# Kernel tuning notes

Measured on AMD Instinct MI355X. Metric: run time of the kernel, lower is better.

The kernel has to match this reference:

```python
import jax, jax.numpy as jnp
import numpy as np

N = 10000      # nodes
E = 100000     # edges
C = 32         # in_channels == hidden_channels == out_channels
ED = 4         # edge_dim
G = 64         # number of graphs in the batch
EPS = 1e-5     # BatchNorm eps


def setup_inputs() -> dict:
    key = jax.random.key(0)
    ks = jax.random.split(key, 20)
    rn = lambda k, shape, s=0.05: jax.random.normal(k, shape, dtype=jnp.float32) * s
    return {
        "x": jax.random.normal(ks[0], (N, C), dtype=jnp.float32),
        "edge_attr": jax.random.normal(ks[1], (E, ED), dtype=jnp.float32),
        # edge MLP 1: ED -> C -> C*C ; NNConv1 root/bias
        "e1_w1": rn(ks[2], (ED, C)), "e1_b1": jnp.zeros((C,), jnp.float32),
        "e1_w2": rn(ks[3], (C, C * C)), "e1_b2": jnp.zeros((C * C,), jnp.float32),
        "root1": rn(ks[4], (C, C)), "bias1": jnp.zeros((C,), jnp.float32),
        # edge MLP 2: ED -> C -> C*C ; NNConv2 root/bias
        "e2_w1": rn(ks[5], (ED, C)), "e2_b1": jnp.zeros((C,), jnp.float32),
        "e2_w2": rn(ks[6], (C, C * C)), "e2_b2": jnp.zeros((C * C,), jnp.float32),
        "root2": rn(ks[7], (C, C)), "bias2": jnp.zeros((C,), jnp.float32),
        # BatchNorm (eval mode: running stats)
        "bn1_g": jnp.ones((C,), jnp.float32), "bn1_b": jnp.zeros((C,), jnp.float32),
        "bn1_m": rn(ks[8], (C,), 0.1), "bn1_v": 1.0 + 0.1 * jax.random.uniform(ks[9], (C,), dtype=jnp.float32),
        "bn2_g": jnp.ones((C,), jnp.float32), "bn2_b": jnp.zeros((C,), jnp.float32),
        "bn2_m": rn(ks[10], (C,), 0.1), "bn2_v": 1.0 + 0.1 * jax.random.uniform(ks[11], (C,), dtype=jnp.float32),
        # readout: C -> C//2 -> 1
        "r1_w": rn(ks[12], (C, C // 2)), "r1_b": jnp.zeros((C // 2,), jnp.float32),
        "r2_w": rn(ks[13], (C // 2, 1)), "r2_b": jnp.zeros((1,), jnp.float32),
        "edge_index": jax.random.randint(ks[14], (2, E), 0, N),
        "batch": jnp.sort(jax.random.randint(ks[15], (N,), 0, G)),
    }


def _nnconv(x, edge_index, edge_attr, w1, b1, w2, b2, root, bias):
    # edge MLP -> per-edge weight matrix [E, C, C]
    h = jax.nn.relu(edge_attr @ w1 + b1)
    W = (h @ w2 + b2).reshape(E, C, C)
    src, dst = edge_index[0], edge_index[1]
    # gather source features, per-edge matmul, scatter-mean to target nodes
    msg = jnp.einsum('ei,eio->eo', x[src], W)                      # [E, C]
    agg = jax.ops.segment_sum(msg, dst, num_segments=N)            # [N, C]
    cnt = jax.ops.segment_sum(jnp.ones((E,), x.dtype), dst, num_segments=N)
    agg = agg / jnp.maximum(cnt, 1.0)[:, None]
    return agg + x @ root + bias


def _bn(x, g, b, m, v):
    return (x - m) * jax.lax.rsqrt(v + EPS) * g + b


def reference(x, edge_attr,
              e1_w1, e1_b1, e1_w2, e1_b2, root1, bias1,
              e2_w1, e2_b1, e2_w2, e2_b2, root2, bias2,
              bn1_g, bn1_b, bn1_m, bn1_v,
              bn2_g, bn2_b, bn2_m, bn2_v,
              r1_w, r1_b, r2_w, r2_b,
              edge_index, batch):
    h = jax.nn.relu(_bn(_nnconv(x, edge_index, edge_attr, e1_w1, e1_b1, e1_w2, e1_b2, root1, bias1),
                        bn1_g, bn1_b, bn1_m, bn1_v))
    h = jax.nn.relu(_bn(_nnconv(h, edge_index, edge_attr, e2_w1, e2_b1, e2_w2, e2_b2, root2, bias2),
                        bn2_g, bn2_b, bn2_m, bn2_v))
    # global mean pool over graphs
    psum = jax.ops.segment_sum(h, batch, num_segments=G)           # [G, C]
    pcnt = jax.ops.segment_sum(jnp.ones((N,), h.dtype), batch, num_segments=G)
    pooled = psum / jnp.maximum(pcnt, 1.0)[:, None]
    # readout MLP (dropout is identity in eval)
    return jax.nn.relu(pooled @ r1_w + r1_b) @ r2_w + r2_b          # [G, 1]
```

## Files before the change

kernel.cpp:

```cpp
#include <hip/hip_runtime.h>

#define NN 10000
#define EE 100000
#define GG 64
#define EPSV 1e-5f
#define SLOTS 1056
#define PST 36
#define PNODE (32*PST)
#define HBLK 391
#define WBLK 160
#define NBK 1250

#define OFF_W2R1   0
#define OFF_W2R2   135168
#define OFF_MSG1   270336
#define OFF_MSG2   13070336
#define OFF_EACSR  25870336
#define OFF_CNT    27470336
#define OFF_DEG    27510336
#define OFF_PSUM   27550336
#define OFF_DONE   27558528
#define OFF_XMID   27558592
#define OFF_ROWPTR 28838592
#define OFF_CURSOR 28878656
#define OFF_COLPTR 28918656
#define OFF_CCUR   28958720
#define OFF_MSRC   28998720
#define OFF_CPOS   29398720

__global__ __launch_bounds__(256) void k_pre(const int* __restrict__ ei,
        int* __restrict__ cnt, int* __restrict__ deg,
        const float* __restrict__ w2a, const float* __restrict__ b2a,
        const float* __restrict__ w2b, const float* __restrict__ b2b,
        float* __restrict__ w2r1, float* __restrict__ w2r2) {
    int blk = blockIdx.x;
    int t = threadIdx.x;
    if (blk < HBLK) {
        int e = blk * 256 + t;
        if (e < EE) {
            atomicAdd(&cnt[ei[EE + e]], 1);
            atomicAdd(&deg[ei[e]], 1);
        }
    } else {
        int b2i = blk - HBLK;
        int s = (b2i % 5) * 256 + t;
        int i = b2i / 5;
        if (s < SLOTS) {
            float va = (s < 1024) ? w2a[(s >> 5) * 1024 + i * 32 + (s & 31)]
                                  : b2a[i * 32 + (s - 1024)];
            float vb = (s < 1024) ? w2b[(s >> 5) * 1024 + i * 32 + (s & 31)]
                                  : b2b[i * 32 + (s - 1024)];
            w2r1[i * SLOTS + s] = va;
            w2r2[i * SLOTS + s] = vb;
        }
    }
}

__global__ __launch_bounds__(1024) void k_scan2(const int* __restrict__ deg,
                                                const int* __restrict__ cnt,
                                                int* __restrict__ rowptr,
                                                int* __restrict__ cursor,
                                                int* __restrict__ colptr,
                                                int* __restrict__ ccursor) {
    __shared__ int buf[1024];
    int pass = blockIdx.x;
    const int* src = pass ? cnt : deg;
    int* dst_p = pass ? colptr : rowptr;
    int* dst_c = pass ? ccursor : cursor;
    int t = threadIdx.x;
    int base = t * 10;
    int v[10]; int s = 0;
    #pragma unroll
    for (int k = 0; k < 10; k++) {
        int idx = base + k;
        v[k] = (idx < NN) ? src[idx] : 0;
        s += v[k];
    }
    buf[t] = s;
    for (int off = 1; off < 1024; off <<= 1) {
        __syncthreads();
        int val = buf[t] + ((t >= off) ? buf[t - off] : 0);
        __syncthreads();
        buf[t] = val;
    }
    __syncthreads();
    int carry = (t > 0) ? buf[t - 1] : 0;
    #pragma unroll
    for (int k = 0; k < 10; k++) {
        int idx = base + k;
        if (idx < NN) { dst_p[idx] = carry; dst_c[idx] = carry; }
        carry += v[k];
    }
    if (t == 1023) dst_p[NN] = buf[1023];
}

__global__ void k_scatter(const int* __restrict__ ei,
        const float* __restrict__ edge_attr,
        int* __restrict__ cursor, int* __restrict__ ccursor,
        int* __restrict__ msrc, int* __restrict__ cpos,
        float4* __restrict__ ea_csr) {
    int e = blockIdx.x * 256 + threadIdx.x;
    if (e >= EE) return;
    int sn = ei[e];
    int dn = ei[EE + e];
    float4 a = *(const float4*)&edge_attr[(size_t)e * 4];
    int pos = atomicAdd(&cursor[sn], 1);
    msrc[pos] = sn;
    ea_csr[pos] = a;
    int cp = atomicAdd(&ccursor[dn], 1);
    cpos[cp] = pos;
}

__global__ __launch_bounds__(256, 3) void k_f1(const float* __restrict__ x,
        const float4* __restrict__ ea_csr,
        const float* __restrict__ w1, const float* __restrict__ b1,
        const float* __restrict__ w2r,
        const int* __restrict__ msrc, const int* __restrict__ rowptr,
        float* __restrict__ msg) {
    __shared__ float xs[8][32];
    __shared__ float P2[8 * PNODE];
    __shared__ float shx[8][32];
    int t = threadIdx.x;
    int o = t & 31;
    int cb = 4 * (t >> 5);
    int n0 = blockIdx.x * 8;

    int ebase = rowptr[n0];
    int eend  = rowptr[n0 + 8];
    int grp = t >> 5;

    float wc0 = w1[o], wc1 = w1[32 + o], wc2 = w1[64 + o], wc3 = w1[96 + o];
    float bb  = b1[o];

    int pos = ebase + grp;
    float4 aC = make_float4(0.f, 0.f, 0.f, 0.f);
    int srcC = n0;
    if (pos < eend) { aC = ea_csr[pos]; srcC = msrc[pos]; }

    xs[grp][o] = x[n0 * 32 + t];
    __syncthreads();

    {
        float acc[4][8];
        #pragma unroll
        for (int k = 0; k < 4; k++)
            #pragma unroll
            for (int n = 0; n < 8; n++) acc[k][n] = 0.f;
        #pragma unroll
        for (int j = 0; j < 8; j++) {
            float wk[4][4];
            #pragma unroll
            for (int r = 0; r < 4; r++)
                #pragma unroll
                for (int k = 0; k < 4; k++)
                    wk[r][k] = w2r[(4 * j + r) * SLOTS + (cb + k) * 32 + o];
            #pragma unroll
            for (int n = 0; n < 8; n++) {
                float4 xq = *(const float4*)&xs[n][4 * j];
                #pragma unroll
                for (int k = 0; k < 4; k++)
                    acc[k][n] += xq.x * wk[0][k] + xq.y * wk[1][k]
                               + xq.z * wk[2][k] + xq.w * wk[3][k];
            }
        }
        #pragma unroll
        for (int n = 0; n < 8; n++) {
            float4 st = make_float4(acc[0][n], acc[1][n], acc[2][n], acc[3][n]);
            *(float4*)&P2[n * PNODE + o * PST + cb] = st;
        }
    }
    if (t < 32) {
        float wb[32];
        #pragma unroll
        for (int i = 0; i < 32; i++) wb[i] = w2r[i * SLOTS + 1024 + t];
        #pragma unroll
        for (int n = 0; n < 8; n++) {
            float b = 0.f;
            #pragma unroll
            for (int j = 0; j < 8; j++) {
                float4 xq = *(const float4*)&xs[n][4 * j];
                b += xq.x * wb[4 * j] + xq.y * wb[4 * j + 1]
                   + xq.z * wb[4 * j + 2] + xq.w * wb[4 * j + 3];
            }
            *(float4*)&P2[n * PNODE + t * PST + 32] = make_float4(b, 0.f, 0.f, 0.f);
        }
    }
    __syncthreads();

    while (pos < eend) {
        int pn = pos + 8;
        float4 aN = aC; int srcN = srcC;
        if (pn < eend) { aN = ea_csr[pn]; srcN = msrc[pn]; }
        float h = fmaxf(aC.x * wc0 + aC.y * wc1 + aC.z * wc2 + aC.w * wc3 + bb, 0.f);
        shx[grp][o] = h;
        asm volatile("" ::: "memory");
        const float* Pn = &P2[(srcC - n0) * PNODE + o * PST];
        float m = Pn[32];
        #pragma unroll
        for (int b = 0; b < 8; b++) {
            float4 hx = *(const float4*)&shx[grp][4 * b];
            float4 pq = *(const float4*)&Pn[4 * b];
            m += hx.x * pq.x + hx.y * pq.y + hx.z * pq.z + hx.w * pq.w;
        }
        msg[(size_t)pos * 32 + o] = m;
        asm volatile("" ::: "memory");
        pos = pn; aC = aN; srcC = srcN;
    }
}

__global__ __launch_bounds__(256, 3) void k_mid(const float* __restrict__ x,
        const float* __restrict__ msg1,
        const int* __restrict__ colptr, const int* __restrict__ cpos,
        const float* __restrict__ root1, const float* __restrict__ bias1,
        const float* __restrict__ bn1g, const float* __restrict__ bn1b,
        const float* __restrict__ bn1m, const float* __restrict__ bn1v,
        const float4* __restrict__ ea_csr,
        const float* __restrict__ w1, const float* __restrict__ b1,
        const float* __restrict__ w2r,
        const int* __restrict__ msrc, const int* __restrict__ rowptr,
        float* __restrict__ xmid, float* __restrict__ msg2) {
    __shared__ float xs[8][32];
    __shared__ float P2[8 * PNODE];
    __shared__ float shx[8][32];
    __shared__ float xmid_s[8][32];
    int t = threadIdx.x;
    int o = t & 31;
    int grp = t >> 5;
    int cb = 4 * grp;
    int n0 = blockIdx.x * 8;

    int ebase = rowptr[n0];
    int eend  = rowptr[n0 + 8];

    float wc0 = w1[o], wc1 = w1[32 + o], wc2 = w1[64 + o], wc3 = w1[96 + o];
    float hbb = b1[o];
    int pos = ebase + grp;
    float4 aC = make_float4(0.f, 0.f, 0.f, 0.f);
    int srcC = n0;
    if (pos < eend) { aC = ea_csr[pos]; srcC = msrc[pos]; }

    xs[grp][o] = x[n0 * 32 + t];
    __syncthreads();
    {
        int k = grp, n = n0 + k;
        float rt = bias1[o];
        #pragma unroll
        for (int i = 0; i < 32; i++) rt += xs[k][i] * root1[i * 32 + o];
        int jbase = colptr[n], jend = colptr[n + 1];
        float acc = 0.f;
        for (int jb = jbase; jb < jend; jb += 32) {
            int nrem = jend - jb;
            int lim = (nrem < 32) ? nrem : 32;
            int cv = 0;
            if (o < lim) cv = cpos[jb + o];
            for (int j = 0; j < lim; j += 8) {
                float v[8];
                #pragma unroll
                for (int q = 0; q < 8; q++) {
                    if (j + q < lim) {
                        int cj = __shfl(cv, j + q, 32);
                        v[q] = msg1[(size_t)cj * 32 + o];
                    } else v[q] = 0.f;
                }
                #pragma unroll
                for (int q = 0; q < 8; q++) acc += v[q];
            }
        }
        float a = acc / fmaxf((float)(jend - jbase), 1.f);
        float val = a + rt;
        val = (val - bn1m[o]) * rsqrtf(bn1v[o] + EPSV) * bn1g[o] + bn1b[o];
        val = fmaxf(val, 0.f);
        xmid_s[k][o] = val;
        xmid[(size_t)n * 32 + o] = val;
    }
    __syncthreads();

    {
        float acc[4][8];
        #pragma unroll
        for (int k = 0; k < 4; k++)
            #pragma unroll
            for (int n = 0; n < 8; n++) acc[k][n] = 0.f;
        #pragma unroll
        for (int j = 0; j < 8; j++) {
            float wk[4][4];
            #pragma unroll
            for (int r = 0; r < 4; r++)
                #pragma unroll
                for (int k = 0; k < 4; k++)
                    wk[r][k] = w2r[(4 * j + r) * SLOTS + (cb + k) * 32 + o];
            #pragma unroll
            for (int n = 0; n < 8; n++) {
                float4 xq = *(const float4*)&xmid_s[n][4 * j];
                #pragma unroll
                for (int k = 0; k < 4; k++)
                    acc[k][n] += xq.x * wk[0][k] + xq.y * wk[1][k]
                               + xq.z * wk[2][k] + xq.w * wk[3][k];
            }
        }
        #pragma unroll
        for (int n = 0; n < 8; n++) {
            float4 st = make_float4(acc[0][n], acc[1][n], acc[2][n], acc[3][n]);
            *(float4*)&P2[n * PNODE + o * PST + cb] = st;
        }
    }
    if (t < 32) {
        float wb[32];
        #pragma unroll
        for (int i = 0; i < 32; i++) wb[i] = w2r[i * SLOTS + 1024 + t];
        #pragma unroll
        for (int n = 0; n < 8; n++) {
            float b = 0.f;
            #pragma unroll
            for (int j = 0; j < 8; j++) {
                float4 xq = *(const float4*)&xmid_s[n][4 * j];
                b += xq.x * wb[4 * j] + xq.y * wb[4 * j + 1]
                   + xq.z * wb[4 * j + 2] + xq.w * wb[4 * j + 3];
            }
            *(float4*)&P2[n * PNODE + t * PST + 32] = make_float4(b, 0.f, 0.f, 0.f);
        }
    }
    __syncthreads();

    while (pos < eend) {
        int pn = pos + 8;
        float4 aN = aC; int srcN = srcC;
        if (pn < eend) { aN = ea_csr[pn]; srcN = msrc[pn]; }
        float h = fmaxf(aC.x * wc0 + aC.y * wc1 + aC.z * wc2 + aC.w * wc3 + hbb, 0.f);
        shx[grp][o] = h;
        asm volatile("" ::: "memory");
        const float* Pn = &P2[(srcC - n0) * PNODE + o * PST];
        float m = Pn[32];
        #pragma unroll
        for (int b = 0; b < 8; b++) {
            float4 hx = *(const float4*)&shx[grp][4 * b];
            float4 pq = *(const float4*)&Pn[4 * b];
            m += hx.x * pq.x + hx.y * pq.y + hx.z * pq.z + hx.w * pq.w;
        }
        msg2[(size_t)pos * 32 + o] = m;
        asm volatile("" ::: "memory");
        pos = pn; aC = aN; srcC = srcN;
    }
}

__global__ __launch_bounds__(256) void k_end(const float* __restrict__ xmid,
        const float* __restrict__ msg2,
        const int* __restrict__ colptr, const int* __restrict__ cpos,
        const float* __restrict__ root2, const float* __restrict__ bias2,
        const float* __restrict__ bn2g, const float* __restrict__ bn2b,
        const float* __restrict__ bn2m, const float* __restrict__ bn2v,
        const int* __restrict__ batch, float* __restrict__ psum,
        int* __restrict__ done,
        const float* __restrict__ r1w, const float* __restrict__ r1b,
        const float* __restrict__ r2w, const float* __restrict__ r2b,
        float* __restrict__ out) {
    __shared__ float xs[8][32];
    __shared__ float vals[8][32];
    __shared__ int gb[8];
    __shared__ float rd[2592];
    __shared__ int lastflag;
    int t = threadIdx.x;
    int o = t & 31;
    int grp = t >> 5;
    int n0 = blockIdx.x * 8;

    xs[grp][o] = xmid[(size_t)n0 * 32 + t];
    __syncthreads();
    int k = grp, n = n0 + k;
    float rt = bias2[o];
    #pragma unroll
    for (int i = 0; i < 32; i++) rt += xs[k][i] * root2[i * 32 + o];
    int jbase = colptr[n], jend = colptr[n + 1];
    float acc = 0.f;
    for (int jb = jbase; jb < jend; jb += 32) {
        int nrem = jend - jb;
        int lim = (nrem < 32) ? nrem : 32;
        int cv = 0;
        if (o < lim) cv = cpos[jb + o];
        for (int j = 0; j < lim; j += 8) {
            float v[8];
            #pragma unroll
            for (int q = 0; q < 8; q++) {
                if (j + q < lim) {
                    int cj = __shfl(cv, j + q, 32);
                    v[q] = msg2[(size_t)cj * 32 + o];
                } else v[q] = 0.f;
            }
            #pragma unroll
            for (int q = 0; q < 8; q++) acc += v[q];
        }
    }
    float a = acc / fmaxf((float)(jend - jbase), 1.f);
    float val = a + rt;
    val = (val - bn2m[o]) * rsqrtf(bn2v[o] + EPSV) * bn2g[o] + bn2b[o];
    val = fmaxf(val, 0.f);
    vals[k][o] = val;
    if (o == 0) gb[k] = batch[n];
    __syncthreads();
    if (k == 0) {
        float pacc = vals[0][o];
        int g = gb[0];
        #pragma unroll
        for (int k2 = 1; k2 < 8; k2++) {
            if (gb[k2] == g) pacc += vals[k2][o];
            else {
                atomicAdd(&psum[(size_t)g * 32 + o], pacc);
                g = gb[k2]; pacc = vals[k2][o];
            }
        }
        atomicAdd(&psum[(size_t)g * 32 + o], pacc);
    }
    __syncthreads();

    if (t == 0) {
        __threadfence();
        int old = atomicAdd(done, 1);
        lastflag = (old == NBK - 1);
    }
    __syncthreads();
    if (!lastflag) return;
    __threadfence();

    float* w1s = rd;
    float* b1s = rd + 512;
    float* w2s = rd + 528;
    float* ps  = rd + 544;
    int cnt_g = 0;
    if (t < GG) {
        int lo = 0, hi = NN;
        while (lo < hi) { int m2 = (lo + hi) >> 1; if (batch[m2] < t) lo = m2 + 1; else hi = m2; }
        int lb = lo;
        lo = 0; hi = NN;
        while (lo < hi) { int m2 = (lo + hi) >> 1; if (batch[m2] < t + 1) lo = m2 + 1; else hi = m2; }
        cnt_g = lo - lb;
    }
    w1s[t] = r1w[t];
    w1s[t + 256] = r1w[t + 256];
    if (t < 16) { b1s[t] = r1b[t]; w2s[t] = r2w[t]; }
    #pragma unroll
    for (int i = 0; i < GG * 32 / 256; i++)
        ps[t + i * 256] = __hip_atomic_load(&psum[t + i * 256], __ATOMIC_RELAXED,
                                            __HIP_MEMORY_SCOPE_AGENT);
    __syncthreads();
    if (t < GG) {
        float inv = 1.f / fmaxf((float)cnt_g, 1.f);
        float acc2 = r2b[0];
        #pragma unroll
        for (int j = 0; j < 16; j++) {
            float dot = 0.f;
            #pragma unroll
            for (int c = 0; c < 32; c++) dot += ps[t * 32 + c] * w1s[c * 16 + j];
            float z = dot * inv + b1s[j];
            acc2 += fmaxf(z, 0.f) * w2s[j];
        }
        out[t] = acc2;
    }
}

extern "C" void kernel_launch(void* const* d_in, const int* in_sizes, int n_in,
                              void* d_out, int out_size, void* d_ws, size_t ws_size,
                              hipStream_t stream) {
    const float* x       = (const float*)d_in[0];
    const float* eattr   = (const float*)d_in[1];
    const float* e1_w1   = (const float*)d_in[2];
    const float* e1_b1   = (const float*)d_in[3];
    const float* e1_w2   = (const float*)d_in[4];
    const float* e1_b2   = (const float*)d_in[5];
    const float* root1   = (const float*)d_in[6];
    const float* bias1   = (const float*)d_in[7];
    const float* e2_w1   = (const float*)d_in[8];
    const float* e2_b1   = (const float*)d_in[9];
    const float* e2_w2   = (const float*)d_in[10];
    const float* e2_b2   = (const float*)d_in[11];
    const float* root2   = (const float*)d_in[12];
    const float* bias2   = (const float*)d_in[13];
    const float* bn1_g   = (const float*)d_in[14];
    const float* bn1_b   = (const float*)d_in[15];
    const float* bn1_m   = (const float*)d_in[16];
    const float* bn1_v   = (const float*)d_in[17];
    const float* bn2_g   = (const float*)d_in[18];
    const float* bn2_b   = (const float*)d_in[19];
    const float* bn2_m   = (const float*)d_in[20];
    const float* bn2_v   = (const float*)d_in[21];
    const float* r1_w    = (const float*)d_in[22];
    const float* r1_b    = (const float*)d_in[23];
    const float* r2_w    = (const float*)d_in[24];
    const float* r2_b    = (const float*)d_in[25];
    const int*   ei      = (const int*)d_in[26];
    const int*   batch   = (const int*)d_in[27];

    char* ws = (char*)d_ws;
    float*  w2r1   = (float*) (ws + OFF_W2R1);
    float*  w2r2   = (float*) (ws + OFF_W2R2);
    float*  msg1   = (float*) (ws + OFF_MSG1);
    float*  msg2   = (float*) (ws + OFF_MSG2);
    float4* ea_csr = (float4*)(ws + OFF_EACSR);
    int*    cnt    = (int*)   (ws + OFF_CNT);
    int*    deg    = (int*)   (ws + OFF_DEG);
    float*  psum   = (float*) (ws + OFF_PSUM);
    int*    done   = (int*)   (ws + OFF_DONE);
    float*  xmid   = (float*) (ws + OFF_XMID);
    int*    rowptr = (int*)   (ws + OFF_ROWPTR);
    int*    cursor = (int*)   (ws + OFF_CURSOR);
    int*    colptr = (int*)   (ws + OFF_COLPTR);
    int*    ccursor= (int*)   (ws + OFF_CCUR);
    int*    msrc   = (int*)   (ws + OFF_MSRC);
    int*    cpos   = (int*)   (ws + OFF_CPOS);

    hipMemsetAsync(ws + OFF_CNT, 0, 88256, stream);

    k_pre<<<HBLK + WBLK, 256, 0, stream>>>(ei, cnt, deg,
                                           e1_w2, e1_b2, e2_w2, e2_b2, w2r1, w2r2);
    k_scan2<<<2, 1024, 0, stream>>>(deg, cnt, rowptr, cursor, colptr, ccursor);
    k_scatter<<<(EE + 255) / 256, 256, 0, stream>>>(ei, eattr,
                                                    cursor, ccursor, msrc, cpos,
                                                    ea_csr);

    k_f1<<<NBK, 256, 0, stream>>>(x, ea_csr, e1_w1, e1_b1, w2r1,
                                  msrc, rowptr, msg1);
    k_mid<<<NBK, 256, 0, stream>>>(x, msg1, colptr, cpos, root1, bias1,
                                   bn1_g, bn1_b, bn1_m, bn1_v,
                                   ea_csr, e2_w1, e2_b1, w2r2,
                                   msrc, rowptr, xmid, msg2);
    k_end<<<NBK, 256, 0, stream>>>(xmid, msg2, colptr, cpos, root2, bias2,
                                   bn2_g, bn2_b, bn2_m, bn2_v,
                                   batch, psum, done,
                                   r1_w, r1_b, r2_w, r2_b, (float*)d_out);
}
```

Before: 263.2 us.

## Write edge messages in destination-sorted order to make aggregation contiguous

```diff
diff --git a/kernel.cpp b/kernel.cpp
--- a/kernel.cpp
+++ b/kernel.cpp
@@ -25,8 +25,7 @@
 #define OFF_CURSOR 28878656
 #define OFF_COLPTR 28918656
 #define OFF_CCUR   28958720
-#define OFF_MSRC   28998720
-#define OFF_CPOS   29398720
+#define OFF_META   28998720
 
 __global__ __launch_bounds__(256) void k_pre(const int* __restrict__ ei,
         int* __restrict__ cnt, int* __restrict__ deg,
@@ -97,25 +96,23 @@
 __global__ void k_scatter(const int* __restrict__ ei,
         const float* __restrict__ edge_attr,
         int* __restrict__ cursor, int* __restrict__ ccursor,
-        int* __restrict__ msrc, int* __restrict__ cpos,
-        float4* __restrict__ ea_csr) {
+        int2* __restrict__ meta, float4* __restrict__ ea_csr) {
     int e = blockIdx.x * 256 + threadIdx.x;
     if (e >= EE) return;
     int sn = ei[e];
     int dn = ei[EE + e];
     float4 a = *(const float4*)&edge_attr[(size_t)e * 4];
     int pos = atomicAdd(&cursor[sn], 1);
-    msrc[pos] = sn;
+    int cs  = atomicAdd(&ccursor[dn], 1);
+    meta[pos] = make_int2(sn, cs);
     ea_csr[pos] = a;
-    int cp = atomicAdd(&ccursor[dn], 1);
-    cpos[cp] = pos;
 }
 
 __global__ __launch_bounds__(256, 3) void k_f1(const float* __restrict__ x,
         const float4* __restrict__ ea_csr,
         const float* __restrict__ w1, const float* __restrict__ b1,
         const float* __restrict__ w2r,
-        const int* __restrict__ msrc, const int* __restrict__ rowptr,
+        const int2* __restrict__ meta, const int* __restrict__ rowptr,
         float* __restrict__ msg) {
     __shared__ float xs[8][32];
     __shared__ float P2[8 * PNODE];
@@ -134,8 +131,8 @@
 
     int pos = ebase + grp;
     float4 aC = make_float4(0.f, 0.f, 0.f, 0.f);
-    int srcC = n0;
-    if (pos < eend) { aC = ea_csr[pos]; srcC = msrc[pos]; }
+    int2 mC = make_int2(n0, 0);
+    if (pos < eend) { aC = ea_csr[pos]; mC = meta[pos]; }
 
     xs[grp][o] = x[n0 * 32 + t];
     __syncthreads();
@@ -189,12 +186,12 @@
 
     while (pos < eend) {
         int pn = pos + 8;
-        float4 aN = aC; int srcN = srcC;
-        if (pn < eend) { aN = ea_csr[pn]; srcN = msrc[pn]; }
+        float4 aN = aC; int2 mN = mC;
+        if (pn < eend) { aN = ea_csr[pn]; mN = meta[pn]; }
         float h = fmaxf(aC.x * wc0 + aC.y * wc1 + aC.z * wc2 + aC.w * wc3 + bb, 0.f);
         shx[grp][o] = h;
         asm volatile("" ::: "memory");
-        const float* Pn = &P2[(srcC - n0) * PNODE + o * PST];
+        const float* Pn = &P2[(mC.x - n0) * PNODE + o * PST];
         float m = Pn[32];
         #pragma unroll
         for (int b = 0; b < 8; b++) {
@@ -202,22 +199,22 @@
             float4 pq = *(const float4*)&Pn[4 * b];
             m += hx.x * pq.x + hx.y * pq.y + hx.z * pq.z + hx.w * pq.w;
         }
-        msg[(size_t)pos * 32 + o] = m;
+        msg[(size_t)mC.y * 32 + o] = m;
         asm volatile("" ::: "memory");
-        pos = pn; aC = aN; srcC = srcN;
+        pos = pn; aC = aN; mC = mN;
     }
 }
 
 __global__ __launch_bounds__(256, 3) void k_mid(const float* __restrict__ x,
         const float* __restrict__ msg1,
-        const int* __restrict__ colptr, const int* __restrict__ cpos,
+        const int* __restrict__ colptr,
         const float* __restrict__ root1, const float* __restrict__ bias1,
         const float* __restrict__ bn1g, const float* __restrict__ bn1b,
         const float* __restrict__ bn1m, const float* __restrict__ bn1v,
         const float4* __restrict__ ea_csr,
         const float* __restrict__ w1, const float* __restrict__ b1,
         const float* __restrict__ w2r,
-        const int* __restrict__ msrc, const int* __restrict__ rowptr,
+        const int2* __restrict__ meta, const int* __restrict__ rowptr,
         float* __restrict__ xmid, float* __restrict__ msg2) {
     __shared__ float xs[8][32];
     __shared__ float P2[8 * PNODE];
@@ -236,8 +233,8 @@
     float hbb = b1[o];
     int pos = ebase + grp;
     float4 aC = make_float4(0.f, 0.f, 0.f, 0.f);
-    int srcC = n0;
-    if (pos < eend) { aC = ea_csr[pos]; srcC = msrc[pos]; }
+    int2 mC = make_int2(n0, 0);
+    if (pos < eend) { aC = ea_csr[pos]; mC = meta[pos]; }
 
     xs[grp][o] = x[n0 * 32 + t];
     __syncthreads();
@@ -248,24 +245,19 @@
         for (int i = 0; i < 32; i++) rt += xs[k][i] * root1[i * 32 + o];
         int jbase = colptr[n], jend = colptr[n + 1];
         float acc = 0.f;
-        for (int jb = jbase; jb < jend; jb += 32) {
-            int nrem = jend - jb;
-            int lim = (nrem < 32) ? nrem : 32;
-            int cv = 0;
-            if (o < lim) cv = cpos[jb + o];
-            for (int j = 0; j < lim; j += 8) {
-                float v[8];
-                #pragma unroll
-                for (int q = 0; q < 8; q++) {
-                    if (j + q < lim) {
-                        int cj = __shfl(cv, j + q, 32);
-                        v[q] = msg1[(size_t)cj * 32 + o];
-                    } else v[q] = 0.f;
-                }
-                #pragma unroll
-                for (int q = 0; q < 8; q++) acc += v[q];
-            }
-        }
+        int j = jbase;
+        for (; j + 8 <= jend; j += 8) {
+            float v0 = msg1[(size_t)(j + 0) * 32 + o];
+            float v1 = msg1[(size_t)(j + 1) * 32 + o];
+            float v2 = msg1[(size_t)(j + 2) * 32 + o];
+            float v3 = msg1[(size_t)(j + 3) * 32 + o];
+            float v4 = msg1[(size_t)(j + 4) * 32 + o];
+            float v5 = msg1[(size_t)(j + 5) * 32 + o];
+            float v6 = msg1[(size_t)(j + 6) * 32 + o];
+            float v7 = msg1[(size_t)(j + 7) * 32 + o];
+            acc += ((v0 + v1) + (v2 + v3)) + ((v4 + v5) + (v6 + v7));
+        }
+        for (; j < jend; j++) acc += msg1[(size_t)j * 32 + o];
         float a = acc / fmaxf((float)(jend - jbase), 1.f);
         float val = a + rt;
         val = (val - bn1m[o]) * rsqrtf(bn1v[o] + EPSV) * bn1g[o] + bn1b[o];
@@ -324,12 +316,12 @@
 
     while (pos < eend) {
         int pn = pos + 8;
-        float4 aN = aC; int srcN = srcC;
-        if (pn < eend) { aN = ea_csr[pn]; srcN = msrc[pn]; }
+        float4 aN = aC; int2 mN = mC;
+        if (pn < eend) { aN = ea_csr[pn]; mN = meta[pn]; }
         float h = fmaxf(aC.x * wc0 + aC.y * wc1 + aC.z * wc2 + aC.w * wc3 + hbb, 0.f);
         shx[grp][o] = h;
         asm volatile("" ::: "memory");
-        const float* Pn = &P2[(srcC - n0) * PNODE + o * PST];
+        const float* Pn = &P2[(mC.x - n0) * PNODE + o * PST];
         float m = Pn[32];
         #pragma unroll
         for (int b = 0; b < 8; b++) {
@@ -337,15 +329,15 @@
             float4 pq = *(const float4*)&Pn[4 * b];
             m += hx.x * pq.x + hx.y * pq.y + hx.z * pq.z + hx.w * pq.w;
         }
-        msg2[(size_t)pos * 32 + o] = m;
+        msg2[(size_t)mC.y * 32 + o] = m;
         asm volatile("" ::: "memory");
-        pos = pn; aC = aN; srcC = srcN;
+        pos = pn; aC = aN; mC = mN;
     }
 }
 
 __global__ __launch_bounds__(256) void k_end(const float* __restrict__ xmid,
         const float* __restrict__ msg2,
-        const int* __restrict__ colptr, const int* __restrict__ cpos,
+        const int* __restrict__ colptr,
         const float* __restrict__ root2, const float* __restrict__ bias2,
         const float* __restrict__ bn2g, const float* __restrict__ bn2b,
         const float* __restrict__ bn2m, const float* __restrict__ bn2v,
@@ -372,24 +364,19 @@
     for (int i = 0; i < 32; i++) rt += xs[k][i] * root2[i * 32 + o];
     int jbase = colptr[n], jend = colptr[n + 1];
     float acc = 0.f;
-    for (int jb = jbase; jb < jend; jb += 32) {
-        int nrem = jend - jb;
-        int lim = (nrem < 32) ? nrem : 32;
-        int cv = 0;
-        if (o < lim) cv = cpos[jb + o];
-        for (int j = 0; j < lim; j += 8) {
-            float v[8];
-            #pragma unroll
-            for (int q = 0; q < 8; q++) {
-                if (j + q < lim) {
-                    int cj = __shfl(cv, j + q, 32);
-                    v[q] = msg2[(size_t)cj * 32 + o];
-                } else v[q] = 0.f;
-            }
-            #pragma unroll
-            for (int q = 0; q < 8; q++) acc += v[q];
-        }
-    }
+    int j = jbase;
+    for (; j + 8 <= jend; j += 8) {
+        float v0 = msg2[(size_t)(j + 0) * 32 + o];
+        float v1 = msg2[(size_t)(j + 1) * 32 + o];
+        float v2 = msg2[(size_t)(j + 2) * 32 + o];
+        float v3 = msg2[(size_t)(j + 3) * 32 + o];
+        float v4 = msg2[(size_t)(j + 4) * 32 + o];
+        float v5 = msg2[(size_t)(j + 5) * 32 + o];
+        float v6 = msg2[(size_t)(j + 6) * 32 + o];
+        float v7 = msg2[(size_t)(j + 7) * 32 + o];
+        acc += ((v0 + v1) + (v2 + v3)) + ((v4 + v5) + (v6 + v7));
+    }
+    for (; j < jend; j++) acc += msg2[(size_t)j * 32 + o];
     float a = acc / fmaxf((float)(jend - jbase), 1.f);
     float val = a + rt;
     val = (val - bn2m[o]) * rsqrtf(bn2v[o] + EPSV) * bn2g[o] + bn2b[o];
@@ -446,12 +433,12 @@
         float inv = 1.f / fmaxf((float)cnt_g, 1.f);
         float acc2 = r2b[0];
         #pragma unroll
-        for (int j = 0; j < 16; j++) {
+        for (int jj = 0; jj < 16; jj++) {
             float dot = 0.f;
             #pragma unroll
-            for (int c = 0; c < 32; c++) dot += ps[t * 32 + c] * w1s[c * 16 + j];
-            float z = dot * inv + b1s[j];
-            acc2 += fmaxf(z, 0.f) * w2s[j];
+            for (int c = 0; c < 32; c++) dot += ps[t * 32 + c] * w1s[c * 16 + jj];
+            float z = dot * inv + b1s[jj];
+            acc2 += fmaxf(z, 0.f) * w2s[jj];
         }
         out[t] = acc2;
     }
@@ -504,8 +491,7 @@
     int*    cursor = (int*)   (ws + OFF_CURSOR);
     int*    colptr = (int*)   (ws + OFF_COLPTR);
     int*    ccursor= (int*)   (ws + OFF_CCUR);
-    int*    msrc   = (int*)   (ws + OFF_MSRC);
-    int*    cpos   = (int*)   (ws + OFF_CPOS);
+    int2*   meta   = (int2*)  (ws + OFF_META);
 
     hipMemsetAsync(ws + OFF_CNT, 0, 88256, stream);
 
@@ -513,16 +499,15 @@
                                            e1_w2, e1_b2, e2_w2, e2_b2, w2r1, w2r2);
     k_scan2<<<2, 1024, 0, stream>>>(deg, cnt, rowptr, cursor, colptr, ccursor);
     k_scatter<<<(EE + 255) / 256, 256, 0, stream>>>(ei, eattr,
-                                                    cursor, ccursor, msrc, cpos,
-                                                    ea_csr);
+                                                    cursor, ccursor, meta, ea_csr);
 
     k_f1<<<NBK, 256, 0, stream>>>(x, ea_csr, e1_w1, e1_b1, w2r1,
-                                  msrc, rowptr, msg1);
-    k_mid<<<NBK, 256, 0, stream>>>(x, msg1, colptr, cpos, root1, bias1,
+                                  meta, rowptr, msg1);
+    k_mid<<<NBK, 256, 0, stream>>>(x, msg1, colptr, root1, bias1,
                                    bn1_g, bn1_b, bn1_m, bn1_v,
                                    ea_csr, e2_w1, e2_b1, w2r2,
-                                   msrc, rowptr, xmid, msg2);
-    k_end<<<NBK, 256, 0, stream>>>(xmid, msg2, colptr, cpos, root2, bias2,
+                                   meta, rowptr, xmid, msg2);
+    k_end<<<NBK, 256, 0, stream>>>(xmid, msg2, colptr, root2, bias2,
                                    bn2_g, bn2_b, bn2_m, bn2_v,
                                    batch, psum, done,
                                    r1_w, r1_b, r2_w, r2_b, (float*)d_out);
```

Result: no change. 261.7 us (-0.6%).
